# Kernel tuning notes

Measured on AMD Instinct MI355X. Metric: run time of the kernel, lower is better.

The kernel has to match this reference:

```python
import jax, jax.numpy as jnp
import numpy as np

EDGES = np.array([[0,6],[0,5],[6,8],[5,7],[0,62],[62,63],[63,64],[59,64],[59,60],[60,61],[61,62],[0,74],[71,72],[72,73],[73,74],[74,75],[75,76],[76,77],[77,78],[78,79],[79,80],[80,81],[81,82],[71,82],[71,83],[77,87],[83,84],[84,85],[85,86],[86,87],[87,88],[88,89],[89,90],[83,90],[0,65],[65,66],[66,67],[67,68],[68,69],[69,70],[65,70],[7,91],[91,92],[92,93],[93,94],[94,95],[91,96],[96,97],[97,98],[98,99],[91,100],[100,101],[101,102],[102,103],[91,104],[104,105],[105,106],[106,107],[91,108],[108,109],[109,110],[110,111],[8,112],[112,113],[113,114],[114,115],[115,116],[112,117],[117,118],[118,119],[119,120],[112,121],[121,122],[122,123],[123,124],[112,125],[125,126],[126,127],[127,128],[112,129],[129,130],[130,131],[131,132]], dtype=np.int32)
N_NODES = 102


def _gcn_structure():
    # Keep only edges whose endpoints fit in the 102-node feature view,
    # add self-loops, and compute symmetric GCN normalization (PyG gcn_norm).
    keep = (EDGES[:, 0] < N_NODES) & (EDGES[:, 1] < N_NODES)
    e = EDGES[keep]
    row, col = e[:, 0], e[:, 1]
    loops = np.arange(N_NODES, dtype=np.int32)
    row_f = np.concatenate([row, loops])
    col_f = np.concatenate([col, loops])
    deg = np.zeros(N_NODES, dtype=np.float32)
    np.add.at(deg, col_f, 1.0)  # in-degree incl. self-loop
    dinv = 1.0 / np.sqrt(np.maximum(deg, 1.0))
    norm = (dinv[row_f] * dinv[col_f]).astype(np.float32)
    return row_f, col_f, norm

_ROW, _COL, _NORM = _gcn_structure()


def setup_inputs() -> dict:
    key = jax.random.key(0)
    ks = jax.random.split(key, 5)
    B = 8192
    return {
        "x": jax.random.normal(ks[0], (B, 204), dtype=jnp.float32),
        "W_gcn": jax.random.normal(ks[1], (2, 64), dtype=jnp.float32) * 0.5,
        "b_gcn": jax.random.normal(ks[2], (64,), dtype=jnp.float32) * 0.1,
        "W_proj": jax.random.normal(ks[3], (64, 128), dtype=jnp.float32) * 0.1,
        "b_proj": jax.random.normal(ks[4], (128,), dtype=jnp.float32) * 0.1,
    }


def reference(x, W_gcn, b_gcn, W_proj, b_proj):
    B = x.shape[0]
    xn = x.reshape(B, N_NODES, 2)                      # (B, 102, 2)
    h = jnp.einsum('bni,ih->bnh', xn, W_gcn)           # GCN linear: (B, 102, H)
    norm = jnp.asarray(_NORM)
    msgs = h[:, _ROW, :] * norm[None, :, None]         # gather + normalize: (B, E+N, H)
    agg = jnp.zeros_like(h).at[:, _COL, :].add(msgs)   # scatter-add into targets
    agg = agg + b_gcn                                  # GCN bias
    act = jax.nn.relu(agg)                             # activation
    out = jnp.einsum('bnh,he->bne', act, W_proj) + b_proj  # projection: (B, 102, 128)
    return out
```

## Files before the change

kernel.cpp:

```cpp
#include <hip/hip_runtime.h>
#include <hip/hip_bf16.h>

#define NN   102
#define NE   83
#define NPAD 128

using bf16x8 = __attribute__((ext_vector_type(8))) short;
using f32x4  = __attribute__((ext_vector_type(4))) float;

__device__ __constant__ int EDGES_C[NE * 2] = {
    0,6, 0,5, 6,8, 5,7, 0,62, 62,63, 63,64, 59,64, 59,60, 60,61, 61,62,
    0,74, 71,72, 72,73, 73,74, 74,75, 75,76, 76,77, 77,78, 78,79, 79,80,
    80,81, 81,82, 71,82, 71,83, 77,87, 83,84, 84,85, 85,86, 86,87, 87,88,
    88,89, 89,90, 83,90, 0,65, 65,66, 66,67, 67,68, 68,69, 69,70, 65,70,
    7,91, 91,92, 92,93, 93,94, 94,95, 91,96, 96,97, 97,98, 98,99, 91,100,
    100,101, 101,102, 102,103, 91,104, 104,105, 105,106, 106,107, 91,108,
    108,109, 109,110, 110,111, 8,112, 112,113, 113,114, 114,115, 115,116,
    112,117, 117,118, 118,119, 119,120, 112,121, 121,122, 122,123, 123,124,
    112,125, 125,126, 126,127, 127,128, 112,129, 129,130, 130,131, 131,132
};

#define WS_BFRAG 0
#define WS_OFF   16384
#define WS_ER    (16384 + 512)
#define WS_EN    (16384 + 512 + 1024)

__device__ inline unsigned short f2bf(float f) {
  union { float f; unsigned u; } v; v.f = f;
  unsigned r = v.u + 0x7fffu + ((v.u >> 16) & 1u);
  return (unsigned short)(r >> 16);
}

__device__ inline unsigned cvt_pk_bf16(float lo, float hi) {
  unsigned r;
  asm("v_cvt_pk_bf16_f32 %0, %1, %2" : "=v"(r) : "v"(lo), "v"(hi));
  return r;
}

__global__ void gnn_setup(const float* __restrict__ Wp, char* __restrict__ ws) {
  const int t = threadIdx.x;

  if (blockIdx.x != 0) {
    unsigned short* bf = (unsigned short*)(ws + WS_BFRAG);
    for (int idx = t; idx < 16 * 64; idx += 256) {
      int lane = idx & 63;
      int f    = idx >> 6;
      int mt   = f >> 1, kc = f & 1;
      int e    = mt * 16 + (lane & 15);
      int kb   = kc * 32 + (lane >> 4) * 8;
      unsigned short* dst = bf + idx * 8;
#pragma unroll
      for (int i = 0; i < 8; ++i) dst[i] = f2bf(Wp[(kb + i) * 128 + e]);
    }
    return;
  }

  __shared__ float s_dinv[NN];
  __shared__ int   s_cnt[NN];
  __shared__ int   s_off[NN + 1];

  if (t < NN) {
    int deg = 1, cnt = 1;
    for (int e = 0; e < NE; ++e) {
      int r = EDGES_C[2*e], c = EDGES_C[2*e+1];
      if (r < NN && c == t) { ++deg; ++cnt; }
    }
    s_dinv[t] = 1.0f / sqrtf((float)deg);
    s_cnt[t]  = cnt;
  }
  __syncthreads();
  if (t < NN) {
    int o = 0;
    for (int c = 0; c < t; ++c) o += s_cnt[c];
    s_off[t] = o;
    if (t == NN - 1) s_off[NN] = o + s_cnt[t];
  }
  __syncthreads();
  int*   off = (int*)(ws + WS_OFF);
  int*   er  = (int*)(ws + WS_ER);
  float* en  = (float*)(ws + WS_EN);
  if (t < NN) {
    int c = t, pos = s_off[c];
    float dc = s_dinv[c];
    er[pos] = c; en[pos] = dc * dc; ++pos;
    for (int e = 0; e < NE; ++e) {
      int r = EDGES_C[2*e], cc = EDGES_C[2*e+1];
      if (r < NN && cc == c) { er[pos] = r; en[pos] = s_dinv[r] * dc; ++pos; }
    }
    off[c] = s_off[c];
    if (c == 0) off[NN] = s_off[NN];
  }
}

__global__ __launch_bounds__(256) void gnn_main(
    const float* __restrict__ x, const float* __restrict__ Wg,
    const float* __restrict__ bg, const float* __restrict__ bp,
    const char* __restrict__ ws, float* __restrict__ out, int B) {
  const int t    = threadIdx.x;
  const int lane = t & 63;
  const int wv   = t >> 6;
  const int b    = blockIdx.x * 4 + wv;

  __shared__ float swg[128];
  __shared__ float sbg[64];
  __shared__ float sbp[128];
  __shared__ float sxw[4][208];
  __shared__ float syw[4][NPAD][2];
  __shared__ float st[4][16][132];

  if (t < 128) { swg[t] = Wg[t]; sbp[t] = bp[t]; }
  if (t < 64)  sbg[t] = bg[t];
  __syncthreads();

  if (b >= B) return;

  float* sx = sxw[wv];
  float (*sy)[2] = syw[wv];

  if (lane < 51)
    *(f32x4*)&sx[lane * 4] = *(const f32x4*)(x + (size_t)b * 204 + lane * 4);

  {
    const int*   off = (const int*)(ws + WS_OFF);
    const int*   er  = (const int*)(ws + WS_ER);
    const float* en  = (const float*)(ws + WS_EN);
#pragma unroll
    for (int half = 0; half < 2; ++half) {
      const int n = lane + half * 64;
      float y0 = 0.f, y1 = 0.f;
      if (n < NN) {
        int s = off[n], e2 = off[n + 1];
        for (int j = s; j < e2; ++j) {
          int r = er[j]; float w = en[j];
          y0 = fmaf(w, sx[2 * r],     y0);
          y1 = fmaf(w, sx[2 * r + 1], y1);
        }
      }
      sy[n][0] = y0; sy[n][1] = y1;
    }
  }

  const int l15 = lane & 15;
  const int lhi = lane >> 4;
  const int kb  = lhi * 8;
  const int rb  = lhi * 4;
  const int c32 = (lane & 31) * 4;
  const int rhi = lane >> 5;

  const bf16x8* bfr = (const bf16x8*)(ws + WS_BFRAG);
  bf16x8 Apf[8][2];
#pragma unroll
  for (int mt = 0; mt < 8; ++mt) {
    Apf[mt][0] = bfr[(mt * 2 + 0) * 64 + lane];
    Apf[mt][1] = bfr[(mt * 2 + 1) * 64 + lane];
  }
  f32x4 bias[8];
#pragma unroll
  for (int mt = 0; mt < 8; ++mt)
    bias[mt] = *(const f32x4*)&sbp[mt * 16 + rb];

  float* ob = out + (size_t)b * (NN * 128);

  for (int nt = 0; nt < 7; ++nt) {
    const int node = nt * 16 + l15;
    const float y0 = sy[node][0], y1 = sy[node][1];
    bf16x8 Bact[2];
#pragma unroll
    for (int kc = 0; kc < 2; ++kc) {
      float v[8];
#pragma unroll
      for (int i = 0; i < 8; ++i) {
        int h = kc * 32 + kb + i;
        float a = fmaf(y0, swg[h], fmaf(y1, swg[64 + h], sbg[h]));
        v[i] = fmaxf(a, 0.f);
      }
      union { unsigned u[4]; bf16x8 f; } pk;
      pk.u[0] = cvt_pk_bf16(v[0], v[1]);
      pk.u[1] = cvt_pk_bf16(v[2], v[3]);
      pk.u[2] = cvt_pk_bf16(v[4], v[5]);
      pk.u[3] = cvt_pk_bf16(v[6], v[7]);
      Bact[kc] = pk.f;
    }

    f32x4 acc[8];
#pragma unroll
    for (int mt = 0; mt < 8; ++mt) acc[mt] = bias[mt];
#pragma unroll
    for (int mt = 0; mt < 8; ++mt)
#pragma unroll
      for (int kc = 0; kc < 2; ++kc)
        acc[mt] = __builtin_amdgcn_mfma_f32_16x16x32_bf16(
            Apf[mt][kc], Bact[kc], acc[mt], 0, 0, 0);

#pragma unroll
    for (int mt = 0; mt < 8; ++mt)
      *(f32x4*)&st[wv][l15][mt * 16 + rb] = acc[mt];

    const int rows = (nt < 6) ? 16 : (NN - 96);
#pragma unroll
    for (int pass = 0; pass < 8; ++pass) {
      const int n2 = pass * 2 + rhi;
      if (n2 < rows) {
        f32x4 row = *(const f32x4*)&st[wv][n2][c32];
        __builtin_nontemporal_store(row,
            (f32x4*)(ob + (nt * 16 + n2) * 128 + c32));
      }
    }
  }
}

extern "C" void kernel_launch(void* const* d_in, const int* in_sizes, int n_in,
                              void* d_out, int out_size, void* d_ws, size_t ws_size,
                              hipStream_t stream) {
  const float* x  = (const float*)d_in[0];
  const float* Wg = (const float*)d_in[1];
  const float* bg = (const float*)d_in[2];
  const float* Wp = (const float*)d_in[3];
  const float* bp = (const float*)d_in[4];
  float* out = (float*)d_out;
  const int B = in_sizes[0] / 204;

  gnn_setup<<<2, 256, 0, stream>>>(Wp, (char*)d_ws);
  gnn_main<<<(B + 3) / 4, 256, 0, stream>>>(x, Wg, bg, bp, (const char*)d_ws, out, B);
}
```

Baseline: 101.9 us.

## Split projection into column halves to cut registers and LDS, raise occupancy

Result: slower. 150.3 us (+47.5%).

```diff
diff --git a/kernel.cpp b/kernel.cpp
--- a/kernel.cpp
+++ b/kernel.cpp
@@ -92,7 +92,7 @@
   }
 }
 
-__global__ __launch_bounds__(256) void gnn_main(
+__global__ __launch_bounds__(256, 5) void gnn_main(
     const float* __restrict__ x, const float* __restrict__ Wg,
     const float* __restrict__ bg, const float* __restrict__ bp,
     const char* __restrict__ ws, float* __restrict__ out, int B) {
@@ -106,7 +106,7 @@
   __shared__ float sbp[128];
   __shared__ float sxw[4][208];
   __shared__ float syw[4][NPAD][2];
-  __shared__ float st[4][16][132];
+  __shared__ float st[4][16][68];
 
   if (t < 128) { swg[t] = Wg[t]; sbp[t] = bp[t]; }
   if (t < 64)  sbg[t] = bg[t];
@@ -144,21 +144,11 @@
   const int lhi = lane >> 4;
   const int kb  = lhi * 8;
   const int rb  = lhi * 4;
-  const int c32 = (lane & 31) * 4;
-  const int rhi = lane >> 5;
+
+  const f32x4 bph0 = *(const f32x4*)&sbp[l15 * 4];
+  const f32x4 bph1 = *(const f32x4*)&sbp[64 + l15 * 4];
 
   const bf16x8* bfr = (const bf16x8*)(ws + WS_BFRAG);
-  bf16x8 Apf[8][2];
-#pragma unroll
-  for (int mt = 0; mt < 8; ++mt) {
-    Apf[mt][0] = bfr[(mt * 2 + 0) * 64 + lane];
-    Apf[mt][1] = bfr[(mt * 2 + 1) * 64 + lane];
-  }
-  f32x4 bias[8];
-#pragma unroll
-  for (int mt = 0; mt < 8; ++mt)
-    bias[mt] = *(const f32x4*)&sbp[mt * 16 + rb];
-
   float* ob = out + (size_t)b * (NN * 128);
 
   for (int nt = 0; nt < 7; ++nt) {
@@ -182,28 +172,32 @@
       Bact[kc] = pk.f;
     }
 
-    f32x4 acc[8];
-#pragma unroll
-    for (int mt = 0; mt < 8; ++mt) acc[mt] = bias[mt];
-#pragma unroll
-    for (int mt = 0; mt < 8; ++mt)
-#pragma unroll
-      for (int kc = 0; kc < 2; ++kc)
-        acc[mt] = __builtin_amdgcn_mfma_f32_16x16x32_bf16(
-            Apf[mt][kc], Bact[kc], acc[mt], 0, 0, 0);
-
-#pragma unroll
-    for (int mt = 0; mt < 8; ++mt)
-      *(f32x4*)&st[wv][l15][mt * 16 + rb] = acc[mt];
-
     const int rows = (nt < 6) ? 16 : (NN - 96);
-#pragma unroll
-    for (int pass = 0; pass < 8; ++pass) {
-      const int n2 = pass * 2 + rhi;
-      if (n2 < rows) {
-        f32x4 row = *(const f32x4*)&st[wv][n2][c32];
-        __builtin_nontemporal_store(row,
-            (f32x4*)(ob + (nt * 16 + n2) * 128 + c32));
+
+#pragma unroll
+    for (int h = 0; h < 2; ++h) {
+      bf16x8 F[4][2];
+#pragma unroll
+      for (int m = 0; m < 4; ++m) {
+        F[m][0] = bfr[((h * 4 + m) * 2 + 0) * 64 + lane];
+        F[m][1] = bfr[((h * 4 + m) * 2 + 1) * 64 + lane];
+      }
+#pragma unroll
+      for (int m = 0; m < 4; ++m) {
+        f32x4 a = {0.f, 0.f, 0.f, 0.f};
+        a = __builtin_amdgcn_mfma_f32_16x16x32_bf16(F[m][0], Bact[0], a, 0, 0, 0);
+        a = __builtin_amdgcn_mfma_f32_16x16x32_bf16(F[m][1], Bact[1], a, 0, 0, 0);
+        *(f32x4*)&st[wv][l15][m * 16 + rb] = a;
+      }
+#pragma unroll
+      for (int pass = 0; pass < 4; ++pass) {
+        const int n2 = pass * 4 + lhi;
+        if (n2 < rows) {
+          f32x4 row = *(const f32x4*)&st[wv][n2][l15 * 4];
+          row = row + (h ? bph1 : bph0);
+          __builtin_nontemporal_store(row,
+              (f32x4*)(ob + (nt * 16 + n2) * 128 + h * 64 + l15 * 4));
+        }
       }
     }
   }
```

## Split graph aggregation and projection into separate kernels via workspace buffer

Applied to the files above, without the earlier changes.

After: 106.5 us. +4.5%, slower.

```diff
diff --git a/kernel.cpp b/kernel.cpp
--- a/kernel.cpp
+++ b/kernel.cpp
@@ -24,6 +24,7 @@
 #define WS_OFF   16384
 #define WS_ER    (16384 + 512)
 #define WS_EN    (16384 + 512 + 1024)
+#define WS_Y     65536
 
 __device__ inline unsigned short f2bf(float f) {
   union { float f; unsigned u; } v; v.f = f;
@@ -92,7 +93,149 @@
   }
 }
 
-__global__ __launch_bounds__(256) void gnn_main(
+__global__ __launch_bounds__(256) void gnn_y(
+    const float* __restrict__ x, const char* __restrict__ ws,
+    float* __restrict__ yout, int B) {
+  const int t    = threadIdx.x;
+  const int lane = t & 63;
+  const int wv   = t >> 6;
+  const int b    = blockIdx.x * 4 + wv;
+
+  __shared__ int   soff[NN + 2];
+  __shared__ int   ser[256];
+  __shared__ float sen[256];
+  __shared__ float sxw[4][208];
+  __shared__ float syw[4][NPAD][2];
+
+  if (t < NN + 1) soff[t] = ((const int*)(ws + WS_OFF))[t];
+  if (t < 256) {
+    ser[t] = ((const int*)(ws + WS_ER))[t];
+    sen[t] = ((const float*)(ws + WS_EN))[t];
+  }
+  __syncthreads();
+
+  if (b >= B) return;
+
+  float* sx = sxw[wv];
+  if (lane < 51)
+    *(f32x4*)&sx[lane * 4] = *(const f32x4*)(x + (size_t)b * 204 + lane * 4);
+
+#pragma unroll
+  for (int half = 0; half < 2; ++half) {
+    const int n = lane + half * 64;
+    float y0 = 0.f, y1 = 0.f;
+    if (n < NN) {
+      int s = soff[n], e2 = soff[n + 1];
+      for (int j = s; j < e2; ++j) {
+        int r = ser[j]; float w = sen[j];
+        y0 = fmaf(w, sx[2 * r],     y0);
+        y1 = fmaf(w, sx[2 * r + 1], y1);
+      }
+    }
+    syw[wv][n][0] = y0; syw[wv][n][1] = y1;
+  }
+
+  f32x4 v = *(const f32x4*)&syw[wv][lane * 2][0];
+  *(f32x4*)(yout + (size_t)b * 256 + lane * 4) = v;
+}
+
+__global__ __launch_bounds__(256) void gnn_out(
+    const float* __restrict__ yin, const float* __restrict__ Wg,
+    const float* __restrict__ bg, const float* __restrict__ bp,
+    const char* __restrict__ ws, float* __restrict__ out, int B) {
+  const int t    = threadIdx.x;
+  const int lane = t & 63;
+  const int wv   = t >> 6;
+  const int b    = blockIdx.x * 4 + wv;
+
+  __shared__ float swg[128];
+  __shared__ float sbg[64];
+  __shared__ float sbp[128];
+  __shared__ float syw[4][NPAD][2];
+  __shared__ float st[4][16][132];
+
+  if (t < 128) { swg[t] = Wg[t]; sbp[t] = bp[t]; }
+  if (t < 64)  sbg[t] = bg[t];
+  __syncthreads();
+
+  if (b >= B) return;
+
+  {
+    f32x4 v = *(const f32x4*)(yin + (size_t)b * 256 + lane * 4);
+    *(f32x4*)&syw[wv][lane * 2][0] = v;
+  }
+  float (*sy)[2] = syw[wv];
+
+  const int l15 = lane & 15;
+  const int lhi = lane >> 4;
+  const int kb  = lhi * 8;
+  const int rb  = lhi * 4;
+  const int c32 = (lane & 31) * 4;
+  const int rhi = lane >> 5;
+
+  const bf16x8* bfr = (const bf16x8*)(ws + WS_BFRAG);
+  bf16x8 Apf[8][2];
+#pragma unroll
+  for (int mt = 0; mt < 8; ++mt) {
+    Apf[mt][0] = bfr[(mt * 2 + 0) * 64 + lane];
+    Apf[mt][1] = bfr[(mt * 2 + 1) * 64 + lane];
+  }
+  f32x4 bias[8];
+#pragma unroll
+  for (int mt = 0; mt < 8; ++mt)
+    bias[mt] = *(const f32x4*)&sbp[mt * 16 + rb];
+
+  float* ob = out + (size_t)b * (NN * 128);
+
+  for (int nt = 0; nt < 7; ++nt) {
+    const int node = nt * 16 + l15;
+    const float y0 = sy[node][0], y1 = sy[node][1];
+    bf16x8 Bact[2];
+#pragma unroll
+    for (int kc = 0; kc < 2; ++kc) {
+      float v[8];
+#pragma unroll
+      for (int i = 0; i < 8; ++i) {
+        int h = kc * 32 + kb + i;
+        float a = fmaf(y0, swg[h], fmaf(y1, swg[64 + h], sbg[h]));
+        v[i] = fmaxf(a, 0.f);
+      }
+      union { unsigned u[4]; bf16x8 f; } pk;
+      pk.u[0] = cvt_pk_bf16(v[0], v[1]);
+      pk.u[1] = cvt_pk_bf16(v[2], v[3]);
+      pk.u[2] = cvt_pk_bf16(v[4], v[5]);
+      pk.u[3] = cvt_pk_bf16(v[6], v[7]);
+      Bact[kc] = pk.f;
+    }
+
+    f32x4 acc[8];
+#pragma unroll
+    for (int mt = 0; mt < 8; ++mt) acc[mt] = bias[mt];
+#pragma unroll
+    for (int mt = 0; mt < 8; ++mt)
+#pragma unroll
+      for (int kc = 0; kc < 2; ++kc)
+        acc[mt] = __builtin_amdgcn_mfma_f32_16x16x32_bf16(
+            Apf[mt][kc], Bact[kc], acc[mt], 0, 0, 0);
+
+#pragma unroll
+    for (int mt = 0; mt < 8; ++mt)
+      *(f32x4*)&st[wv][l15][mt * 16 + rb] = acc[mt];
+
+    const int rows = (nt < 6) ? 16 : (NN - 96);
+#pragma unroll
+    for (int pass = 0; pass < 8; ++pass) {
+      const int n2 = pass * 2 + rhi;
+      if (n2 < rows) {
+        f32x4 row = *(const f32x4*)&st[wv][n2][c32];
+        __builtin_nontemporal_store(row,
+            (f32x4*)(ob + (nt * 16 + n2) * 128 + c32));
+      }
+    }
+  }
+}
+
+__global__ __launch_bounds__(256) void gnn_fused(
     const float* __restrict__ x, const float* __restrict__ Wg,
     const float* __restrict__ bg, const float* __restrict__ bp,
     const char* __restrict__ ws, float* __restrict__ out, int B) {
@@ -219,7 +362,15 @@
   const float* bp = (const float*)d_in[4];
   float* out = (float*)d_out;
   const int B = in_sizes[0] / 204;
+  const int grid = (B + 3) / 4;
 
   gnn_setup<<<2, 256, 0, stream>>>(Wp, (char*)d_ws);
-  gnn_main<<<(B + 3) / 4, 256, 0, stream>>>(x, Wg, bg, bp, (const char*)d_ws, out, B);
-}
+
+  if (ws_size >= (size_t)WS_Y + (size_t)B * 1024) {
+    float* yws = (float*)((char*)d_ws + WS_Y);
+    gnn_y  <<<grid, 256, 0, stream>>>(x, (const char*)d_ws, yws, B);
+    gnn_out<<<grid, 256, 0, stream>>>(yws, Wg, bg, bp, (const char*)d_ws, out, B);
+  } else {
+    gnn_fused<<<grid, 256, 0, stream>>>(x, Wg, bg, bp, (const char*)d_ws, out, B);
+  }
+}
```
